# Kernel tuning notes

Hardware: AMD Instinct MI355X
Metric: run time of the kernel (lower is better)

The kernel has to match this reference:

```python
import jax, jax.numpy as jnp
import numpy as np

D = 32   # manifold_dim
H = 128  # hidden_dim
B = 32   # batch


def setup_inputs() -> dict:
    key = jax.random.key(0)
    ks = jax.random.split(key, 13)
    def lin(k, fan_in, shape):
        # torch nn.Linear default init: U(-1/sqrt(fan_in), 1/sqrt(fan_in))
        return jax.random.uniform(k, shape, jnp.float32, -1.0, 1.0) / np.float32(np.sqrt(fan_in))
    return {
        "points": jax.random.normal(ks[0], (B, D), jnp.float32),
        # metric_network: Linear(D,H) -> ReLU -> Linear(H, D*D)
        "mw1": lin(ks[1], D, (D, H)), "mb1": lin(ks[2], D, (H,)),
        "mw2": lin(ks[3], H, (H, D * D)), "mb2": lin(ks[4], H, (D * D,)),
        # christoffel_network: Linear(D+3,H) -> Tanh -> Linear(H,1)  (scalar output per (i,j,k))
        "cw1": lin(ks[5], D + 3, (D + 3, H)), "cb1": lin(ks[6], D + 3, (H,)),
        "cw2": lin(ks[7], H, (H,)), "cb2": lin(ks[8], H, ()),
        # ricci_network: Linear(2D+1, 2H) -> ReLU -> Linear(2H, 1)
        "rw1": lin(ks[9], 2 * D + 1, (2 * D + 1, 2 * H)), "rb1": lin(ks[10], 2 * D + 1, (2 * H,)),
        "rw2": lin(ks[11], 2 * H, (2 * H,)), "rb2": lin(ks[12], 2 * H, ()),
    }


def _forward(points, mw1, mb1, mw2, mb2, cw1, cb1, cw2, cb2, rw1, rb1, rw2, rb2):
    b, d = points.shape
    # metric tensor g: [b, d, d]
    metric = (jax.nn.relu(points @ mw1 + mb1) @ mw2 + mb2).reshape(b, d, d)

    # Christoffel MLP input per (i,j,k): cat([points, g_ij, g_jk, g_ki]) -> [b,d,d,d,d+3]
    gij = jnp.broadcast_to(metric[:, :, :, None], (b, d, d, d))                       # g[i,j]
    gjk = jnp.broadcast_to(metric[:, None, :, :], (b, d, d, d))                       # g[j,k]
    gki = jnp.broadcast_to(jnp.swapaxes(metric, 1, 2)[:, :, None, :], (b, d, d, d))   # g[k,i]
    pts = jnp.broadcast_to(points[:, None, None, None, :], (b, d, d, d, d))
    cin = jnp.concatenate([pts, gij[..., None], gjk[..., None], gki[..., None]], axis=-1)
    ch = jnp.tanh(jnp.einsum('bijkf,fh->bijkh', cin, cw1) + cb1)
    christoffel = jnp.einsum('bijkh,h->bijk', ch, cw2) + cb2                          # [b,d,d,d]

    # Ricci MLP input per (i,j): cat([points, g_ij, Gamma_ij[:]]) -> [b,d,d,2d+1]
    pts2 = jnp.broadcast_to(points[:, None, None, :], (b, d, d, d))
    rin = jnp.concatenate([pts2, metric[..., None], christoffel], axis=-1)
    rh = jax.nn.relu(jnp.einsum('bijf,fh->bijh', rin, rw1) + rb1)
    ricci = jnp.einsum('bijh,h->bij', rh, rw2) + rb2                                  # [b,d,d]
    return ricci


def reference(points, mw1, mb1, mw2, mb2, cw1, cb1, cw2, cb2, rw1, rb1, rw2, rb2):
    return _forward(points, mw1, mb1, mw2, mb2, cw1, cb1, cw2, cb2, rw1, rb1, rw2, rb2)
```

## Files before the change

### kernel.cpp

```cpp
#include <hip/hip_runtime.h>

#define D 32
#define H 128

typedef float v2f __attribute__((ext_vector_type(2)));

__global__ __launch_bounds__(256) void setup_kernel(
    const float* __restrict__ points,
    const float* __restrict__ mw1, const float* __restrict__ mb1,
    const float* __restrict__ mw2, const float* __restrict__ mb2,
    const float* __restrict__ cw1, const float* __restrict__ cb1,
    const float* __restrict__ cw2, const float* __restrict__ cb2,
    const float* __restrict__ rw1, const float* __restrict__ rb1,
    float* __restrict__ metric, float4* __restrict__ cpk4,
    float* __restrict__ rbase, float* __restrict__ wm2, float* __restrict__ cc)
{
    __shared__ float p[D];
    __shared__ float h1[H];
    const int b = blockIdx.x;
    const int t = threadIdx.x;
    if (t < D) p[t] = points[b * D + t];
    __syncthreads();

    if (t < H) {
        float acc = mb1[t];
        #pragma unroll
        for (int d = 0; d < D; ++d) acc = fmaf(p[d], mw1[d * H + t], acc);
        h1[t] = fmaxf(acc, 0.0f);

        constexpr float Kc = 2.8853900817779268f;
        float cacc = cb1[t];
        #pragma unroll
        for (int d = 0; d < D; ++d) cacc = fmaf(p[d], cw1[d * H + t], cacc);
        cpk4[b * H + t] = make_float4(Kc * cacc,
                                      Kc * cw1[32 * H + t],
                                      Kc * cw1[33 * H + t],
                                      Kc * cw1[34 * H + t]);
        if (b == 0) wm2[t] = -2.0f * cw2[t];
    }
    {
        float racc = rb1[t];
        #pragma unroll
        for (int d = 0; d < D; ++d) racc = fmaf(p[d], rw1[d * 256 + t], racc);
        rbase[b * 256 + t] = racc;
    }
    if (b == 0 && t < 64) {
        float v = cw2[t] + cw2[t + 64];
        #pragma unroll
        for (int off = 32; off > 0; off >>= 1) v += __shfl_xor(v, off);
        if (t == 0) cc[0] = v + cb2[0];
    }
    __syncthreads();

    #pragma unroll
    for (int q = 0; q < 4; ++q) {
        const int m = q * 256 + t;
        float acc = mb2[m];
        for (int h = 0; h < H; ++h) acc = fmaf(h1[h], mw2[h * 1024 + m], acc);
        metric[b * 1024 + m] = acc;
    }
}

__global__ __launch_bounds__(256) void christoffel_kernel(
    const float* __restrict__ metric,
    const float4* __restrict__ cpk4, const float* __restrict__ wm2,
    const float* __restrict__ cc,
    float* __restrict__ gamma)
{
    __shared__ float M[D * D];
    const int blk = blockIdx.x;
    const int b   = blk >> 6;
    const int i   = (blk >> 1) & 31;
    const int jh  = blk & 1;
    const int t   = threadIdx.x;

    #pragma unroll
    for (int q = 0; q < 4; ++q) M[q * 256 + t] = metric[b * 1024 + q * 256 + t];
    __syncthreads();

    const int j  = jh * 16 + (t >> 4);
    const int k0 = (t & 15) * 2;

    const float gij = M[i * 32 + j];
    const v2f gjk = *(const v2f*)(&M[j * 32 + k0]);
    v2f gki; gki.x = M[k0 * 32 + i]; gki.y = M[(k0 + 1) * 32 + i];
    v2f acc = (v2f)(0.0f);

    const float4* __restrict__ cp = cpk4 + b * H;

    #pragma unroll 4
    for (int h = 0; h < H; ++h) {
        const float4 c  = cp[h];
        const float woh = wm2[h];
        const float pre = fmaf(gij, c.y, c.x);
        v2f x = gjk * c.z + (v2f)(pre);
        x = gki * c.w + x;
        v2f e;
        e.x = __builtin_amdgcn_exp2f(x.x);
        e.y = __builtin_amdgcn_exp2f(x.y);
        e = e + (v2f)(1.0f);
        v2f rc;
        rc.x = __builtin_amdgcn_rcpf(e.x);
        rc.y = __builtin_amdgcn_rcpf(e.y);
        acc = rc * woh + acc;
    }

    const v2f res = acc + (v2f)(cc[0]);
    *((v2f*)(gamma + ((b * 32 + i) * 32 + j) * 32 + k0)) = res;
}

__global__ __launch_bounds__(256) void ricci_kernel(
    const float* __restrict__ metric, const float* __restrict__ rbase,
    const float* __restrict__ rw1, const float* __restrict__ rw2,
    const float* __restrict__ rb2,
    const float* __restrict__ gamma,
    float* __restrict__ out)
{
    __shared__ float red[4][16];
    const int blk = blockIdx.x;
    const int bi  = blk >> 1;
    const int b   = blk >> 6;
    const int i   = (blk >> 1) & 31;
    const int jh  = blk & 1;
    const int t   = threadIdx.x;

    float w[33];
    #pragma unroll
    for (int f = 0; f < 33; ++f) w[f] = rw1[(32 + f) * 256 + t];
    const float rbv   = rbase[b * 256 + t];
    const float wo    = rw2[t];
    const float rbias = rb2[0];

    const float4* __restrict__ G4   = (const float4*)(gamma + bi * 1024 + jh * 512);
    const float*  __restrict__ Mrow = metric + b * 1024 + i * 32 + jh * 16;

    const int wid  = t >> 6;
    const int lane = t & 63;

    #pragma unroll 2
    for (int jp = 0; jp < 8; ++jp) {
        float pp[2];
        #pragma unroll
        for (int s = 0; s < 2; ++s) {
            const int jj = jp * 2 + s;
            v2f hA = (v2f)(0.0f), hB = (v2f)(0.0f);
            #pragma unroll
            for (int k4 = 0; k4 < 8; ++k4) {
                const float4 g = G4[jj * 8 + k4];
                v2f glo; glo.x = g.x; glo.y = g.y;
                v2f ghi; ghi.x = g.z; ghi.y = g.w;
                v2f wlo; wlo.x = w[k4 * 4 + 1]; wlo.y = w[k4 * 4 + 2];
                v2f whi; whi.x = w[k4 * 4 + 3]; whi.y = w[k4 * 4 + 4];
                hA = glo * wlo + hA;
                hB = ghi * whi + hB;
            }
            const float hid = fmaf(Mrow[jj], w[0], rbv) + (hA.x + hA.y) + (hB.x + hB.y);
            pp[s] = fmaxf(hid, 0.0f) * wo;
        }
        const float t0 = pp[0] + __shfl_xor(pp[0], 1);
        const float t1 = pp[1] + __shfl_xor(pp[1], 1);
        float z = (lane & 1) ? t1 : t0;
        #pragma unroll
        for (int off = 2; off < 64; off <<= 1) z += __shfl_xor(z, off);
        if (lane < 2) red[wid][jp * 2 + lane] = z;
    }
    __syncthreads();
    if (t < 16) out[bi * 32 + jh * 16 + t] = red[0][t] + red[1][t] + red[2][t] + red[3][t] + rbias;
}

extern "C" void kernel_launch(void* const* d_in, const int* in_sizes, int n_in,
                              void* d_out, int out_size, void* d_ws, size_t ws_size,
                              hipStream_t stream) {
    const float* points = (const float*)d_in[0];
    const float* mw1 = (const float*)d_in[1];
    const float* mb1 = (const float*)d_in[2];
    const float* mw2 = (const float*)d_in[3];
    const float* mb2 = (const float*)d_in[4];
    const float* cw1 = (const float*)d_in[5];
    const float* cb1 = (const float*)d_in[6];
    const float* cw2 = (const float*)d_in[7];
    const float* cb2 = (const float*)d_in[8];
    const float* rw1 = (const float*)d_in[9];
    const float* rb1 = (const float*)d_in[10];
    const float* rw2 = (const float*)d_in[11];
    const float* rb2 = (const float*)d_in[12];
    float* out = (float*)d_out;

    char* ws = (char*)d_ws;
    float*  metric = (float*)(ws);
    float4* cpk4   = (float4*)(ws + 131072);
    float*  rbase  = (float*)(ws + 196608);
    float*  wm2    = (float*)(ws + 229376);
    float*  cc     = (float*)(ws + 229888);
    float*  gamma  = (float*)(ws + 262144);

    setup_kernel<<<32, 256, 0, stream>>>(points, mw1, mb1, mw2, mb2,
                                         cw1, cb1, cw2, cb2, rw1, rb1,
                                         metric, cpk4, rbase, wm2, cc);
    christoffel_kernel<<<2048, 256, 0, stream>>>(metric, cpk4, wm2, cc, gamma);
    ricci_kernel<<<2048, 256, 0, stream>>>(metric, rbase, rw1, rw2, rb2, gamma, out);
}
```

Measured before the change: 58.53 us.

## Split setup work across more blocks and replace rcp with Newton reciprocal

The setup kernel now launches 8 blocks per batch element. Each block computes one 128-column slice of the metric projection, and the auxiliary precomputations are spread across different block indices. This is meant to fix the severe underuse of the GPU with only 32 blocks. In exchange, the first-layer hidden vector is recomputed in every block. Separately, the Christoffel loop swaps the hardware reciprocal for an integer-magic initial guess refined by two Newton steps, trading one transcendental op for several FMA-rate ops, with a small accuracy risk.

Measured after the change: 55.41 us. -5.3%, faster.

```diff
diff --git a/kernel.cpp b/kernel.cpp
--- a/kernel.cpp
+++ b/kernel.cpp
@@ -17,8 +17,10 @@
 {
     __shared__ float p[D];
     __shared__ float h1[H];
-    const int b = blockIdx.x;
-    const int t = threadIdx.x;
+    const int blk = blockIdx.x;
+    const int b   = blk >> 3;
+    const int q   = blk & 7;
+    const int t   = threadIdx.x;
     if (t < D) p[t] = points[b * D + t];
     __syncthreads();
 
@@ -27,7 +29,9 @@
         #pragma unroll
         for (int d = 0; d < D; ++d) acc = fmaf(p[d], mw1[d * H + t], acc);
         h1[t] = fmaxf(acc, 0.0f);
-
+    }
+
+    if (q == 0 && t < H) {
         constexpr float Kc = 2.8853900817779268f;
         float cacc = cb1[t];
         #pragma unroll
@@ -38,13 +42,13 @@
                                       Kc * cw1[34 * H + t]);
         if (b == 0) wm2[t] = -2.0f * cw2[t];
     }
-    {
+    if (q == 1) {
         float racc = rb1[t];
         #pragma unroll
         for (int d = 0; d < D; ++d) racc = fmaf(p[d], rw1[d * 256 + t], racc);
         rbase[b * 256 + t] = racc;
     }
-    if (b == 0 && t < 64) {
+    if (q == 2 && b == 0 && t < 64) {
         float v = cw2[t] + cw2[t + 64];
         #pragma unroll
         for (int off = 32; off > 0; off >>= 1) v += __shfl_xor(v, off);
@@ -52,10 +56,10 @@
     }
     __syncthreads();
 
-    #pragma unroll
-    for (int q = 0; q < 4; ++q) {
-        const int m = q * 256 + t;
+    if (t < 128) {
+        const int m = q * 128 + t;
         float acc = mb2[m];
+        #pragma unroll 8
         for (int h = 0; h < H; ++h) acc = fmaf(h1[h], mw2[h * 1024 + m], acc);
         metric[b * 1024 + m] = acc;
     }
@@ -95,14 +99,16 @@
         const float pre = fmaf(gij, c.y, c.x);
         v2f x = gjk * c.z + (v2f)(pre);
         x = gki * c.w + x;
-        v2f e;
-        e.x = __builtin_amdgcn_exp2f(x.x);
-        e.y = __builtin_amdgcn_exp2f(x.y);
-        e = e + (v2f)(1.0f);
-        v2f rc;
-        rc.x = __builtin_amdgcn_rcpf(e.x);
-        rc.y = __builtin_amdgcn_rcpf(e.y);
-        acc = rc * woh + acc;
+        v2f y;
+        y.x = __builtin_amdgcn_exp2f(x.x);
+        y.y = __builtin_amdgcn_exp2f(x.y);
+        y = y + (v2f)(1.0f);
+        v2f r;
+        r.x = __uint_as_float(0x7EF311C3u - __float_as_uint(y.x));
+        r.y = __uint_as_float(0x7EF311C3u - __float_as_uint(y.y));
+        r = r * ((v2f)(2.0f) - y * r);
+        r = r * ((v2f)(2.0f) - y * r);
+        acc = r * woh + acc;
     }
 
     const v2f res = acc + (v2f)(cc[0]);
@@ -194,9 +200,9 @@
     float*  cc     = (float*)(ws + 229888);
     float*  gamma  = (float*)(ws + 262144);
 
-    setup_kernel<<<32, 256, 0, stream>>>(points, mw1, mb1, mw2, mb2,
-                                         cw1, cb1, cw2, cb2, rw1, rb1,
-                                         metric, cpk4, rbase, wm2, cc);
+    setup_kernel<<<256, 256, 0, stream>>>(points, mw1, mb1, mw2, mb2,
+                                          cw1, cb1, cw2, cb2, rw1, rb1,
+                                          metric, cpk4, rbase, wm2, cc);
     christoffel_kernel<<<2048, 256, 0, stream>>>(metric, cpk4, wm2, cc, gamma);
     ricci_kernel<<<2048, 256, 0, stream>>>(metric, rbase, rw1, rw2, rb2, gamma, out);
 }
```
